# Performance work log

Hardware: AMD Instinct MI355X
Metric: run time of the kernel (lower is better)

The kernel has to match this reference:

```python
import jax, jax.numpy as jnp
import numpy as np
from jax import lax

N_HEADS = 8
D_K = 64
D_V = 64
TEMP = float(np.sqrt(D_K))  # MixtureOfSoftMax temperature = d_k ** 0.5


def avg_pool_3x3_s2_same(x):
    """TF-style AveragePooling2D(pool=3, stride=2, padding='same'), NHWC.
    TF excludes padded elements from the average (divide by valid count)."""
    sums = lax.reduce_window(x, 0.0, lax.add, (1, 3, 3, 1), (1, 2, 2, 1), 'SAME')
    ones = jnp.ones(x.shape[:3] + (1,), x.dtype)
    cnt = lax.reduce_window(ones, 0.0, lax.add, (1, 3, 3, 1), (1, 2, 2, 1), 'SAME')
    return sums / cnt


def conv1x1(x, w, b):
    # 1x1 conv == per-pixel channel matmul
    return jnp.einsum('bhwc,cd->bhwd', x, w) + b


def setup_inputs() -> dict:
    key = jax.random.key(0)
    ks = jax.random.split(key, 6)
    C = 512
    s1 = float(np.sqrt(2.0 / (C + D_K)))  # init_weight1 std
    s3 = float(np.sqrt(2.0 / (C + D_V)))  # init_weight3 std
    return {
        'x':   jax.random.normal(ks[0], (4, 64, 64, C), jnp.float32),
        'w_q': jax.random.normal(ks[1], (C, N_HEADS * D_K), jnp.float32) * s1,
        'b_q': jnp.zeros((N_HEADS * D_K,), jnp.float32),
        'w_k': jax.random.normal(ks[2], (C, N_HEADS * D_K), jnp.float32) * s1,
        'b_k': jnp.zeros((N_HEADS * D_K,), jnp.float32),
        'w_v': jax.random.normal(ks[3], (C, N_HEADS * D_V), jnp.float32) * s3,
        'b_v': jnp.zeros((N_HEADS * D_V,), jnp.float32),
        'w_o': jax.random.normal(ks[4], (N_HEADS * D_V, C), jnp.float32) * 0.02,
        'b_o': jnp.zeros((C,), jnp.float32),
    }


def reference(x, w_q, b_q, w_k, b_k, w_v, b_v, w_o, b_o):
    BS, H, W, C = x.shape
    residual = x
    # Q from full-res x; K, V from 3x3/s2 average-pooled x (pooling=True)
    qt = conv1x1(x, w_q, b_q).reshape(BS * N_HEADS, H * W, -1)          # (B*h, N, d_k)
    xp = avg_pool_3x3_s2_same(x)                                         # (BS, H/2, W/2, C)
    kt = conv1x1(xp, w_k, b_k).reshape(BS * N_HEADS, H * W // 4, -1)     # (B*h, N/4, d_k)
    vt = conv1x1(xp, w_v, b_v).reshape(BS * N_HEADS, H * W // 4, -1)     # (B*h, N/4, d_v)
    # MixtureOfSoftMaxACF with n_mix=1: scaled dot-product softmax attention
    attn = jnp.einsum('bnd,bmd->bnm', qt, kt) / TEMP                     # (B*h, N, N/4)
    attn = jax.nn.softmax(attn, axis=-1)                                 # dropout=identity (inference)
    out = jnp.einsum('bnm,bmd->bnd', attn, vt)                           # (B*h, N, d_v)
    out = out.reshape(BS, H, W, -1)
    out = conv1x1(out, w_o, b_o)                                         # conv1x1_bn_relu (Conv2D only in call)
    return out + residual                                                # concat=False -> Add
```

## Files before the change

kernel.cpp:

```cpp
#include <hip/hip_runtime.h>
#include <hip/hip_bf16.h>
#include <math.h>

typedef short bf16x8 __attribute__((ext_vector_type(8)));
typedef float f32x4 __attribute__((ext_vector_type(4)));
typedef unsigned short u16;

__device__ inline float b2f(u16 h) {
    unsigned int u = ((unsigned int)h) << 16;
    float f;
    __builtin_memcpy(&f, &u, 4);
    return f;
}

__device__ inline u16 f2b(float f) {
    unsigned int u;
    __builtin_memcpy(&u, &f, 4);
    unsigned int lsb = (u >> 16) & 1u;
    u += 0x7fffu + lsb;
    return (u16)(u >> 16);
}

__device__ __forceinline__ void gl2lds16(const u16* g, u16* l) {
    __builtin_amdgcn_global_load_lds(
        (const __attribute__((address_space(1))) unsigned int*)g,
        (__attribute__((address_space(3))) unsigned int*)l,
        16, 0, 0);
}

#define PITCH 72

#define QSCALE 0.18033688011112042f

__global__ __launch_bounds__(256) void cvtw_kernel(const float* __restrict__ x,
                                                   u16* __restrict__ xb,
                                                   const float* __restrict__ w0,
                                                   const float* __restrict__ w1,
                                                   const float* __restrict__ w2,
                                                   const float* __restrict__ w3,
                                                   u16* __restrict__ wt) {
    __shared__ u16 T[64 * PITCH];
    int tid = threadIdx.x;
    if (blockIdx.x < 8192) {
        int idx = blockIdx.x * 256 + tid;
        float4 v = ((const float4*)x)[idx];
        ushort4 o;
        o.x = f2b(v.x); o.y = f2b(v.y); o.z = f2b(v.z); o.w = f2b(v.w);
        ((ushort4*)xb)[idx] = o;
        return;
    }
    int t5 = blockIdx.x - 8192;
    int bx = t5 & 7, by = (t5 >> 3) & 7, bz = t5 >> 6;
    const float* W = bz == 0 ? w0 : bz == 1 ? w1 : bz == 2 ? w2 : w3;
    u16* WT = wt + (size_t)bz * 262144;
    int nB = bx * 64, kB = by * 64;
#pragma unroll
    for (int t = 0; t < 4; ++t) {
        int e = tid + t * 256;
        int r = e >> 4, c4 = (e & 15) * 4;
        float4 v = *(const float4*)(&W[(size_t)(kB + r) * 512 + nB + c4]);
        u16* dst = &T[r * PITCH + c4];
        dst[0] = f2b(v.x); dst[1] = f2b(v.y); dst[2] = f2b(v.z); dst[3] = f2b(v.w);
    }
    __syncthreads();
    int n = tid & 63, kg = tid >> 6;
#pragma unroll
    for (int p = 0; p < 2; ++p) {
        int k0 = (kg + p * 4) * 8;
        u16 tmp[8];
#pragma unroll
        for (int i = 0; i < 8; ++i) tmp[i] = T[(k0 + i) * PITCH + n];
        *(int4*)(&WT[(size_t)(nB + n) * 512 + kB + k0]) = *(int4*)tmp;
    }
}

__device__ __forceinline__ void pool_body(int idx, const u16* __restrict__ xb,
                                          u16* __restrict__ xp) {
    int c8 = idx & 63;
    int j = (idx >> 6) & 31;
    int i = (idx >> 11) & 31;
    int b = idx >> 16;
    int r0 = 2 * i, c0 = 2 * j;
    int rmax = min(r0 + 3, 64), cmax = min(c0 + 3, 64);
    float acc[8] = {};
    for (int r = r0; r < rmax; ++r)
        for (int cc = c0; cc < cmax; ++cc) {
            bf16x8 v = *(const bf16x8*)(
                &xb[(size_t)((((b << 6) + r) << 6) + cc) * 512 + c8 * 8]);
#pragma unroll
            for (int t = 0; t < 8; ++t) acc[t] += b2f(((const u16*)&v)[t]);
        }
    float inv = 1.f / (float)((rmax - r0) * (cmax - c0));
    u16 o[8];
#pragma unroll
    for (int t = 0; t < 8; ++t) o[t] = f2b(acc[t] * inv);
    *(int4*)(&xp[(size_t)idx * 8]) = *(int4*)o;
}

template <int OM, int BN, int GY>
__device__ __forceinline__ void gemm_body(int bid,
                                          const u16* __restrict__ A,
                                          const u16* __restrict__ WT,
                                          const float* __restrict__ bias,
                                          const float* __restrict__ bias2res,
                                          void* __restrict__ Cv,
                                          void* __restrict__ Cv2,
                                          float oscale,
                                          u16* At, u16* Bt) {
    int tid = threadIdx.x, lane = tid & 63, wave = tid >> 6;
    int q = lane >> 4, l16 = lane & 15;
    constexpr int MI = (BN == 128) ? 2 : 1;
    int wm, wn;
    if constexpr (BN == 128) { wm = wave & 1; wn = wave >> 1; }
    else                     { wm = wave;     wn = 0; }
    int nBlk = bid / GY;
    int mBlk = bid - nBlk * GY;
    int nBase = nBlk * BN, mBase = mBlk * 64;
    f32x4 acc[MI][4] = {};

    for (int kk = 0; kk < 512; kk += 64) {
        __syncthreads();
#pragma unroll
        for (int t = 0; t < 2; ++t) {
            int c = tid + t * 256;
            int m = c >> 3, kc = (c & 7) ^ (m & 7);
            gl2lds16(&A[(size_t)(mBase + m) * 512 + kk + kc * 8], &At[c * 8]);
        }
#pragma unroll
        for (int t = 0; t < BN / 32; ++t) {
            int c = tid + t * 256;
            int m = c >> 3, kc = (c & 7) ^ (m & 7);
            gl2lds16(&WT[(size_t)(nBase + m) * 512 + kk + kc * 8], &Bt[c * 8]);
        }
        __syncthreads();
#pragma unroll
        for (int ds = 0; ds < 2; ++ds) {
            bf16x8 a[MI], b[4];
#pragma unroll
            for (int i = 0; i < MI; ++i) {
                int ma = (BN == 128 ? wm * 32 : wm * 16) + i * 16 + l16;
                a[i] = *(bf16x8*)(&At[ma * 64 + ((((ds << 2) + q) ^ (ma & 7)) << 3)]);
            }
#pragma unroll
            for (int j = 0; j < 4; ++j) {
                int nb = wn * 64 + j * 16 + l16;
                b[j] = *(bf16x8*)(&Bt[nb * 64 + ((((ds << 2) + q) ^ (nb & 7)) << 3)]);
            }
#pragma unroll
            for (int i = 0; i < MI; ++i)
#pragma unroll
                for (int j = 0; j < 4; ++j)
                    acc[i][j] = __builtin_amdgcn_mfma_f32_16x16x32_bf16(a[i], b[j], acc[i][j], 0, 0, 0);
        }
    }

    bool isK = (OM != 3) || (nBase < 512);
#pragma unroll
    for (int j = 0; j < 4; ++j) {
        int col = nBase + wn * 64 + j * 16 + l16;
        float bv;
        if constexpr (OM == 3) bv = isK ? bias[col] : bias2res[col - 512];
        else bv = bias[col];
#pragma unroll
        for (int i = 0; i < MI; ++i) {
#pragma unroll
            for (int r = 0; r < 4; ++r) {
                int row = mBase + (BN == 128 ? wm * 32 : wm * 16) + i * 16 + q * 4 + r;
                float v = acc[i][j][r] + bv;
                if constexpr (OM == 1) {
                    v += bias2res[(size_t)row * 512 + col];
                    ((float*)Cv)[(size_t)row * 512 + col] = v;
                } else if constexpr (OM == 0) {
                    ((u16*)Cv)[(size_t)row * 512 + col] = f2b(v * oscale);
                } else {
                    if (isK) {
                        ((u16*)Cv)[(size_t)row * 512 + col] = f2b(v);
                    } else {
                        int colv = col - 512;
                        int g = row >> 7, m2 = ((row & 127) << 3) + (colv >> 6), d = colv & 63;
                        ((u16*)Cv2)[(size_t)((g << 6) + d) * 1024 + m2] = f2b(v);
                    }
                }
            }
        }
    }
}

__global__ __launch_bounds__(256, 4) void qpool_kernel(const u16* __restrict__ xb,
                                                       const u16* __restrict__ wTq,
                                                       const float* __restrict__ b_q,
                                                       u16* __restrict__ Qw,
                                                       u16* __restrict__ xp) {
    __shared__ __align__(16) u16 At[64 * 64];
    __shared__ __align__(16) u16 Bt[128 * 64];
    int gid = blockIdx.x;
    if (gid < 1024) {
        gemm_body<0, 128, 256>(gid, xb, wTq, b_q, nullptr, Qw, nullptr, QSCALE, At, Bt);
    } else {
        pool_body((gid - 1024) * 256 + threadIdx.x, xb, xp);
    }
}

__global__ __launch_bounds__(256, 4) void gemm_kv_kernel(const u16* __restrict__ xp,
                                                         const u16* __restrict__ wTkv,
                                                         const float* __restrict__ b_k,
                                                         const float* __restrict__ b_v,
                                                         u16* __restrict__ Kw,
                                                         u16* __restrict__ VwT) {
    __shared__ __align__(16) u16 At[64 * 64];
    __shared__ __align__(16) u16 Bt[64 * 64];
    gemm_body<3, 64, 64>(blockIdx.x, xp, wTkv, b_k, b_v, Kw, VwT, 1.0f, At, Bt);
}

__global__ __launch_bounds__(256, 4) void gemm_o_kernel(const u16* __restrict__ Ow,
                                                        const u16* __restrict__ wTo,
                                                        const float* __restrict__ b_o,
                                                        const float* __restrict__ xres,
                                                        float* __restrict__ out) {
    __shared__ __align__(16) u16 At[64 * 64];
    __shared__ __align__(16) u16 Bt[128 * 64];
    gemm_body<1, 128, 256>(blockIdx.x, Ow, wTo, b_o, xres, out, nullptr, 1.0f, At, Bt);
}

__global__ __launch_bounds__(256, 4) void attn_kernel(const u16* __restrict__ Q,
                                                      const u16* __restrict__ K,
                                                      const u16* __restrict__ VT_g,
                                                      u16* __restrict__ O) {
    int g = blockIdx.x;
    int qtile = blockIdx.y;
    const u16* Qg = Q + (size_t)g * 262144;
    const u16* Kg = K + (size_t)g * 65536;
    const u16* Vt = VT_g + (size_t)g * 65536;
    u16* Og = O + (size_t)g * 262144;

    __shared__ __align__(16) u16 Kt[2][64 * 64];
    __shared__ __align__(16) u16 VTs[2][64 * 64];
    __shared__ __align__(16) u16 Pt[64 * 64];

    int tid = threadIdx.x, lane = tid & 63, wave = tid >> 6;
    int q = lane >> 4, l16 = lane & 15;
    int n0 = qtile * 128;
    int pkey = (l16 & 7) << 2;
    int prow = (wave * 16 + l16) * 32;
    int* Pt32 = (int*)Pt;

    bf16x8 qf[2][2];
#pragma unroll
    for (int s = 0; s < 2; ++s)
#pragma unroll
        for (int ds = 0; ds < 2; ++ds)
            qf[s][ds] = *(const bf16x8*)(
                &Qg[(size_t)(n0 + s * 64 + wave * 16 + l16) * 64 + ds * 32 + q * 8]);

    f32x4 oacc[2][4] = {};
    float rsum[2] = {0.f, 0.f};

    auto stage = [&](int buf, int kb) {
#pragma unroll
        for (int t = 0; t < 2; ++t) {
            int c = tid + t * 256;
            int m = c >> 3, kc = (c & 7) ^ (m & 7);
            gl2lds16(&Kg[(size_t)(kb * 64 + m) * 64 + kc * 8], &Kt[buf][c * 8]);
            gl2lds16(&Vt[(size_t)m * 1024 + kb * 64 + kc * 8], &VTs[buf][c * 8]);
        }
    };

    stage(0, 0);
    asm volatile("s_waitcnt vmcnt(0)" ::: "memory");
    __syncthreads();

    int cur = 0;
#pragma unroll 1
    for (int kb = 0; kb < 16; ++kb) {
        if (kb < 15) stage(cur ^ 1, kb + 1);
        const u16* KtB = Kt[cur];
        const u16* VTsB = VTs[cur];
#pragma unroll
        for (int s = 0; s < 2; ++s) {
#pragma unroll
            for (int cb = 0; cb < 4; ++cb) {
                int m = cb * 16 + l16;
                bf16x8 kf0 = *(const bf16x8*)(&KtB[m * 64 + ((q ^ (m & 7)) << 3)]);
                bf16x8 kf1 = *(const bf16x8*)(&KtB[m * 64 + (((4 + q) ^ (m & 7)) << 3)]);
                f32x4 z = {};
                __builtin_amdgcn_s_setprio(1);
                z = __builtin_amdgcn_mfma_f32_16x16x32_bf16(kf0, qf[s][0], z, 0, 0, 0);
                z = __builtin_amdgcn_mfma_f32_16x16x32_bf16(kf1, qf[s][1], z, 0, 0, 0);
                __builtin_amdgcn_s_setprio(0);
                float p0 = __builtin_amdgcn_exp2f(z[0]);
                float p1 = __builtin_amdgcn_exp2f(z[1]);
                float p2 = __builtin_amdgcn_exp2f(z[2]);
                float p3 = __builtin_amdgcn_exp2f(z[3]);
                rsum[s] += (p0 + p1) + (p2 + p3);
                unsigned w0, w1;
                asm("v_cvt_pk_bf16_f32 %0, %1, %2" : "=v"(w0) : "v"(p0), "v"(p1));
                asm("v_cvt_pk_bf16_f32 %0, %1, %2" : "=v"(w1) : "v"(p2), "v"(p3));
                int2 w;
                w.x = (int)w0;
                w.y = (int)w1;
                int pd = (cb * 8 + q * 2) ^ pkey;
                *(int2*)(&Pt32[prow + pd]) = w;
            }
#pragma unroll
            for (int ds = 0; ds < 2; ++ds) {
                int pd = (ds * 16 + q * 4) ^ pkey;
                bf16x8 ap = *(bf16x8*)(&Pt32[prow + pd]);
                __builtin_amdgcn_s_setprio(1);
#pragma unroll
                for (int db = 0; db < 4; ++db) {
                    int dd = db * 16 + l16;
                    int jj = ds * 4 + q;
                    bf16x8 vb = *(const bf16x8*)(&VTsB[dd * 64 + ((jj ^ (dd & 7)) << 3)]);
                    oacc[s][db] = __builtin_amdgcn_mfma_f32_16x16x32_bf16(ap, vb, oacc[s][db], 0, 0, 0);
                }
                __builtin_amdgcn_s_setprio(0);
            }
        }
        asm volatile("s_waitcnt vmcnt(0)" ::: "memory");
        __syncthreads();
        cur ^= 1;
    }

#pragma unroll
    for (int s = 0; s < 2; ++s) {
        float v = rsum[s];
        v += __shfl_xor(v, 16, 64);
        v += __shfl_xor(v, 32, 64);
        rsum[s] = v;
    }
    float inv[2][4];
#pragma unroll
    for (int s = 0; s < 2; ++s)
#pragma unroll
        for (int r = 0; r < 4; ++r)
            inv[s][r] = 1.f / __shfl(rsum[s], q * 4 + r, 64);
#pragma unroll
    for (int s = 0; s < 2; ++s)
#pragma unroll
        for (int db = 0; db < 4; ++db)
#pragma unroll
            for (int r = 0; r < 4; ++r) {
                int row = n0 + s * 64 + wave * 16 + q * 4 + r;
                Og[(size_t)row * 64 + db * 16 + l16] = f2b(oacc[s][db][r] * inv[s][r]);
            }
}

extern "C" void kernel_launch(void* const* d_in, const int* in_sizes, int n_in,
                              void* d_out, int out_size, void* d_ws, size_t ws_size,
                              hipStream_t stream) {
    const float* x   = (const float*)d_in[0];
    const float* w_q = (const float*)d_in[1];
    const float* b_q = (const float*)d_in[2];
    const float* w_k = (const float*)d_in[3];
    const float* b_k = (const float*)d_in[4];
    const float* w_v = (const float*)d_in[5];
    const float* b_v = (const float*)d_in[6];
    const float* w_o = (const float*)d_in[7];
    const float* b_o = (const float*)d_in[8];
    float* out = (float*)d_out;

    char* ws = (char*)d_ws;
    u16* xb  = (u16*)(ws);
    u16* xp  = (u16*)(ws + (16ull << 20));
    u16* Qw  = (u16*)(ws + (20ull << 20));
    u16* Kw  = (u16*)(ws + (36ull << 20));
    u16* VwT = (u16*)(ws + (40ull << 20));
    u16* wT  = (u16*)(ws + (44ull << 20));
    u16* Ow  = xb;

    cvtw_kernel<<<8448, 256, 0, stream>>>(x, xb, w_q, w_k, w_v, w_o, wT);
    qpool_kernel<<<2048, 256, 0, stream>>>(xb, wT, b_q, Qw, xp);
    gemm_kv_kernel<<<1024, 256, 0, stream>>>(xp, wT + 262144, b_k, b_v, Kw, VwT);
    attn_kernel<<<dim3(32, 32), 256, 0, stream>>>(Qw, Kw, VwT, Ow);
    gemm_o_kernel<<<1024, 256, 0, stream>>>(Ow, wT + 786432, b_o, x, out);
}
```

Baseline: 201.6 us.

## Fuse pooling into prep kernel and merge Q and KV projections into one launch

Average pooling now runs inside the conversion/prep kernel and reads the fp32 input directly, instead of reading the bf16 copy inside the Q-projection launch. This lets the Q projection and the K/V projection GEMMs share a single 2048-block launch, removing one launch boundary and letting the two GEMMs overlap. The attention launch is split into two half-grid launches over query tiles. The costs are that pooling now reads twice the bytes (fp32 instead of bf16), and the attention split adds a launch with no clear benefit on its own.

```diff
diff --git a/kernel.cpp b/kernel.cpp
--- a/kernel.cpp
+++ b/kernel.cpp
@@ -32,13 +32,14 @@
 
 #define QSCALE 0.18033688011112042f
 
-__global__ __launch_bounds__(256) void cvtw_kernel(const float* __restrict__ x,
+__global__ __launch_bounds__(256) void prep_kernel(const float* __restrict__ x,
                                                    u16* __restrict__ xb,
                                                    const float* __restrict__ w0,
                                                    const float* __restrict__ w1,
                                                    const float* __restrict__ w2,
                                                    const float* __restrict__ w3,
-                                                   u16* __restrict__ wt) {
+                                                   u16* __restrict__ wt,
+                                                   u16* __restrict__ xp) {
     __shared__ u16 T[64 * PITCH];
     int tid = threadIdx.x;
     if (blockIdx.x < 8192) {
@@ -49,6 +50,30 @@
         ((ushort4*)xb)[idx] = o;
         return;
     }
+    if (blockIdx.x >= 8448) {
+        int idx = (blockIdx.x - 8448) * 256 + tid;
+        int c8 = idx & 63;
+        int j = (idx >> 6) & 31;
+        int i = (idx >> 11) & 31;
+        int b = idx >> 16;
+        int r0 = 2 * i, c0 = 2 * j;
+        int rmax = min(r0 + 3, 64), cmax = min(c0 + 3, 64);
+        float acc[8] = {};
+        for (int r = r0; r < rmax; ++r)
+            for (int cc = c0; cc < cmax; ++cc) {
+                const float* p = &x[(size_t)((((b << 6) + r) << 6) + cc) * 512 + c8 * 8];
+                float4 v0 = *(const float4*)p;
+                float4 v1 = *(const float4*)(p + 4);
+                acc[0] += v0.x; acc[1] += v0.y; acc[2] += v0.z; acc[3] += v0.w;
+                acc[4] += v1.x; acc[5] += v1.y; acc[6] += v1.z; acc[7] += v1.w;
+            }
+        float inv = 1.f / (float)((rmax - r0) * (cmax - c0));
+        u16 o[8];
+#pragma unroll
+        for (int t = 0; t < 8; ++t) o[t] = f2b(acc[t] * inv);
+        *(int4*)(&xp[(size_t)idx * 8]) = *(int4*)o;
+        return;
+    }
     int t5 = blockIdx.x - 8192;
     int bx = t5 & 7, by = (t5 >> 3) & 7, bz = t5 >> 6;
     const float* W = bz == 0 ? w0 : bz == 1 ? w1 : bz == 2 ? w2 : w3;
@@ -72,29 +97,6 @@
         for (int i = 0; i < 8; ++i) tmp[i] = T[(k0 + i) * PITCH + n];
         *(int4*)(&WT[(size_t)(nB + n) * 512 + kB + k0]) = *(int4*)tmp;
     }
-}
-
-__device__ __forceinline__ void pool_body(int idx, const u16* __restrict__ xb,
-                                          u16* __restrict__ xp) {
-    int c8 = idx & 63;
-    int j = (idx >> 6) & 31;
-    int i = (idx >> 11) & 31;
-    int b = idx >> 16;
-    int r0 = 2 * i, c0 = 2 * j;
-    int rmax = min(r0 + 3, 64), cmax = min(c0 + 3, 64);
-    float acc[8] = {};
-    for (int r = r0; r < rmax; ++r)
-        for (int cc = c0; cc < cmax; ++cc) {
-            bf16x8 v = *(const bf16x8*)(
-                &xb[(size_t)((((b << 6) + r) << 6) + cc) * 512 + c8 * 8]);
-#pragma unroll
-            for (int t = 0; t < 8; ++t) acc[t] += b2f(((const u16*)&v)[t]);
-        }
-    float inv = 1.f / (float)((rmax - r0) * (cmax - c0));
-    u16 o[8];
-#pragma unroll
-    for (int t = 0; t < 8; ++t) o[t] = f2b(acc[t] * inv);
-    *(int4*)(&xp[(size_t)idx * 8]) = *(int4*)o;
 }
 
 template <int OM, int BN, int GY>
@@ -186,30 +188,23 @@
     }
 }
 
-__global__ __launch_bounds__(256, 4) void qpool_kernel(const u16* __restrict__ xb,
-                                                       const u16* __restrict__ wTq,
-                                                       const float* __restrict__ b_q,
-                                                       u16* __restrict__ Qw,
-                                                       u16* __restrict__ xp) {
+__global__ __launch_bounds__(256, 4) void qkv_kernel(const u16* __restrict__ xb,
+                                                     const u16* __restrict__ xp,
+                                                     const u16* __restrict__ wT,
+                                                     const float* __restrict__ b_q,
+                                                     const float* __restrict__ b_k,
+                                                     const float* __restrict__ b_v,
+                                                     u16* __restrict__ Qw,
+                                                     u16* __restrict__ Kw,
+                                                     u16* __restrict__ VwT) {
     __shared__ __align__(16) u16 At[64 * 64];
     __shared__ __align__(16) u16 Bt[128 * 64];
     int gid = blockIdx.x;
     if (gid < 1024) {
-        gemm_body<0, 128, 256>(gid, xb, wTq, b_q, nullptr, Qw, nullptr, QSCALE, At, Bt);
+        gemm_body<0, 128, 256>(gid, xb, wT, b_q, nullptr, Qw, nullptr, QSCALE, At, Bt);
     } else {
-        pool_body((gid - 1024) * 256 + threadIdx.x, xb, xp);
-    }
-}
-
-__global__ __launch_bounds__(256, 4) void gemm_kv_kernel(const u16* __restrict__ xp,
-                                                         const u16* __restrict__ wTkv,
-                                                         const float* __restrict__ b_k,
-                                                         const float* __restrict__ b_v,
-                                                         u16* __restrict__ Kw,
-                                                         u16* __restrict__ VwT) {
-    __shared__ __align__(16) u16 At[64 * 64];
-    __shared__ __align__(16) u16 Bt[64 * 64];
-    gemm_body<3, 64, 64>(blockIdx.x, xp, wTkv, b_k, b_v, Kw, VwT, 1.0f, At, Bt);
+        gemm_body<3, 64, 64>(gid - 1024, xp, wT + 262144, b_k, b_v, Kw, VwT, 1.0f, At, Bt);
+    }
 }
 
 __global__ __launch_bounds__(256, 4) void gemm_o_kernel(const u16* __restrict__ Ow,
@@ -225,9 +220,10 @@
 __global__ __launch_bounds__(256, 4) void attn_kernel(const u16* __restrict__ Q,
                                                       const u16* __restrict__ K,
                                                       const u16* __restrict__ VT_g,
-                                                      u16* __restrict__ O) {
+                                                      u16* __restrict__ O,
+                                                      int qt0) {
     int g = blockIdx.x;
-    int qtile = blockIdx.y;
+    int qtile = qt0 + blockIdx.y;
     const u16* Qg = Q + (size_t)g * 262144;
     const u16* Kg = K + (size_t)g * 65536;
     const u16* Vt = VT_g + (size_t)g * 65536;
@@ -368,9 +364,9 @@
     u16* wT  = (u16*)(ws + (44ull << 20));
     u16* Ow  = xb;
 
-    cvtw_kernel<<<8448, 256, 0, stream>>>(x, xb, w_q, w_k, w_v, w_o, wT);
-    qpool_kernel<<<2048, 256, 0, stream>>>(xb, wT, b_q, Qw, xp);
-    gemm_kv_kernel<<<1024, 256, 0, stream>>>(xp, wT + 262144, b_k, b_v, Kw, VwT);
-    attn_kernel<<<dim3(32, 32), 256, 0, stream>>>(Qw, Kw, VwT, Ow);
+    prep_kernel<<<9472, 256, 0, stream>>>(x, xb, w_q, w_k, w_v, w_o, wT, xp);
+    qkv_kernel<<<2048, 256, 0, stream>>>(xb, xp, wT, b_q, b_k, b_v, Qw, Kw, VwT);
+    attn_kernel<<<dim3(32, 16), 256, 0, stream>>>(Qw, Kw, VwT, Ow, 0);
+    attn_kernel<<<dim3(32, 16), 256, 0, stream>>>(Qw, Kw, VwT, Ow, 16);
     gemm_o_kernel<<<1024, 256, 0, stream>>>(Ow, wT + 786432, b_o, x, out);
 }
```

After: 214.9 us. 6.6% more time.
